# Kernel tuning notes

Hardware: AMD Instinct MI355X
Metric: run time of the kernel (lower is better)

Reference implementation:

```python
import jax, jax.numpy as jnp
import numpy as np

V, E, H, DV = 32000, 512, 1024, 512
B, K = 64, 49


def setup_inputs():
    key = jax.random.key(0)
    ks = jax.random.split(key, 16)
    p = lambda i, shape: jax.random.normal(ks[i], shape, dtype=jnp.float32) * 0.02
    return {
        "thought": jax.random.normal(ks[0], (B, H), dtype=jnp.float32),
        "visual_features": jax.random.normal(ks[1], (B, K, DV), dtype=jnp.float32),
        "max_len": 64,
        "embedding": p(2, (V, E)),
        "Wih1": p(3, (4 * H, E)), "Whh1": p(4, (4 * H, H)),
        "bih1": jnp.zeros((4 * H,), jnp.float32), "bhh1": jnp.zeros((4 * H,), jnp.float32),
        "Wih2": p(5, (4 * H, H)), "Whh2": p(6, (4 * H, H)),
        "bih2": jnp.zeros((4 * H,), jnp.float32), "bhh2": jnp.zeros((4 * H,), jnp.float32),
        "Wg1": p(7, (H, H)), "bg1": jnp.zeros((H,), jnp.float32),
        "Wg2": p(8, (1, H)), "bg2": jnp.zeros((1,), jnp.float32),
        "Wo": p(9, (V, H)), "bo": jnp.zeros((V,), jnp.float32),
        "Wv": p(10, (H, DV)), "bv": jnp.zeros((H,), jnp.float32),
        "ln_g": jnp.ones((H,), jnp.float32), "ln_b": jnp.zeros((H,), jnp.float32),
    }


def _lstm_cell(x, h, c, Wih, Whh, bih, bhh):
    # PyTorch LSTM gate order: i, f, g, o
    z = x @ Wih.T + h @ Whh.T + bih + bhh
    i, f, g, o = jnp.split(z, 4, axis=-1)
    c_new = jax.nn.sigmoid(f) * c + jax.nn.sigmoid(i) * jnp.tanh(g)
    h_new = jax.nn.sigmoid(o) * jnp.tanh(c_new)
    return h_new, c_new


def reference(thought, visual_features, max_len, embedding, Wih1, Whh1, bih1, bhh1,
              Wih2, Whh2, bih2, bbh2=None, bih2_dummy=None, **_unused):
    raise RuntimeError('placeholder')


def reference(thought, visual_features, max_len, embedding, Wih1, Whh1, bih1, bhh1,
              Wih2, Whh2, bih2, bhh2, Wg1, bg1, Wg2, bg2, Wo, bo, Wv, bv, ln_g, ln_b):
    Bsz, Hd = thought.shape
    temperature = 0.4  # epoch = 0 -> 0.4 + 0.4*0
    top_p = 0.7        # epoch = 0 -> 0.7 + 0.2*0
    scale = 1.0 / jnp.sqrt(jnp.asarray(Hd, jnp.float32))
    # visual_proj: Linear + LayerNorm (Dropout is identity in eval mode)
    vp = visual_features @ Wv.T + bv
    mu = vp.mean(-1, keepdims=True)
    var = vp.var(-1, keepdims=True)
    vp = (vp - mu) / jnp.sqrt(var + 1e-5) * ln_g + ln_b  # [B,K,H]
    b_idx = jnp.arange(Bsz)
    # carry: (h1,c1,h2,c2, input token, last-3 token history, history validity)
    init = (thought, jnp.zeros_like(thought), thought, jnp.zeros_like(thought),
            jnp.full((Bsz,), 1, jnp.int32),
            jnp.zeros((Bsz, 3), jnp.int32), jnp.zeros((Bsz, 3), jnp.bool_))
    keys = jax.random.split(jax.random.key(42), max_len)

    def step(carry, key):
        h1, c1, h2, c2, inp, hist, histv = carry
        emb = embedding[inp]  # [B,E]
        h1, c1 = _lstm_cell(emb, h1, c1, Wih1, Whh1, bih1, bhh1)
        h2, c2 = _lstm_cell(h1, h2, c2, Wih2, Whh2, bih2, bhh2)
        gate = jax.nn.sigmoid(jnp.tanh(h2 @ Wg1.T + bg1) @ Wg2.T + bg2)  # [B,1]
        out = h2 * gate
        attn = jax.nn.softmax(jnp.einsum('bh,bkh->bk', out, vp) * scale, axis=-1)
        out = out + jnp.einsum('bk,bkh->bh', attn, vp)
        logits = out @ Wo.T + bo  # [B,V]
        # repetition penalty: -2.0 once per UNIQUE token in last-3 history (set semantics via .max)
        pen = jnp.zeros_like(logits).at[b_idx[:, None], hist].max(histv.astype(logits.dtype))
        logits = (logits - 2.0 * pen) / temperature
        # nucleus (top-p) filtering, matching top_k_top_p_filtering with top_k=0
        order = jnp.argsort(-logits, axis=-1)
        sl = jnp.take_along_axis(logits, order, axis=-1)
        cum = jnp.cumsum(jax.nn.softmax(sl, axis=-1), axis=-1)
        rem = cum > top_p
        rem = jnp.concatenate([jnp.zeros_like(rem[:, :1]), rem[:, :-1]], axis=-1)
        mask = jnp.zeros_like(rem).at[b_idx[:, None], order].set(rem)
        logits = jnp.where(mask, -jnp.inf, logits)
        nxt = jax.random.categorical(key, logits).astype(jnp.int32)  # multinomial sample
        hist = jnp.concatenate([hist[:, 1:], nxt[:, None]], axis=1)
        histv = jnp.concatenate([histv[:, 1:], jnp.ones((Bsz, 1), jnp.bool_)], axis=1)
        return (h1, c1, h2, c2, nxt, hist, histv), nxt

    _, toks = jax.lax.scan(step, init, keys)
    return toks.T  # [B, max_len]
```

## Files before the change

### kernel.cpp

```cpp
#include <hip/hip_runtime.h>
#include <hip/hip_bf16.h>
#include <stdint.h>


#define B_   64
#define H_   1024
#define E_   512
#define DV_  512
#define KV_  49
#define V_   32000
#define T_   64

__device__ __forceinline__ uint32_t rotl32(uint32_t x, int r) {
  return (x << r) | (x >> (32 - r));
}
__device__ __forceinline__ void tf2x32(uint32_t k0, uint32_t k1,
                                       uint32_t x0, uint32_t x1,
                                       uint32_t& o0, uint32_t& o1) {
  uint32_t ks0 = k0, ks1 = k1, ks2 = k0 ^ k1 ^ 0x1BD11BDAu;
  x0 += ks0; x1 += ks1;
#define RND_(r) { x0 += x1; x1 = rotl32(x1, r) ^ x0; }
  RND_(13) RND_(15) RND_(26) RND_(6)  x0 += ks1; x1 += ks2 + 1u;
  RND_(17) RND_(29) RND_(16) RND_(24) x0 += ks2; x1 += ks0 + 2u;
  RND_(13) RND_(15) RND_(26) RND_(6)  x0 += ks0; x1 += ks1 + 3u;
  RND_(17) RND_(29) RND_(16) RND_(24) x0 += ks1; x1 += ks2 + 4u;
  RND_(13) RND_(15) RND_(26) RND_(6)  x0 += ks2; x1 += ks0 + 5u;
#undef RND_
  o0 = x0; o1 = x1;
}

__device__ __forceinline__ unsigned key_of(float f) {
  unsigned u = __float_as_uint(f);
  return (u & 0x80000000u) ? ~u : (u | 0x80000000u);
}
__device__ __forceinline__ float sigf(float x) { return 1.0f / (1.0f + expf(-x)); }

template <int BN, int TM, int TN, int NTHR>
__global__ __launch_bounds__(NTHR)
void gemm_dq(const float* __restrict__ A0, int lda0, const float* __restrict__ W0,
             int ldw0, int K0, float* __restrict__ out0, int ldo0, int nt0,
             const float* __restrict__ A1, int lda1, const float* __restrict__ W1,
             int ldw1, int K1, float* __restrict__ out1, int ldo1) {
  constexpr int LD = 36;
  constexpr int ROWS = 64 + BN;
  constexpr int NF4 = ROWS * 8 / NTHR;
  constexpr int BUFST = ROWS * LD;
  constexpr int CG = BN / TN;
  static_assert(ROWS * 8 % NTHR == 0, "staging divisibility");
  static_assert((64 / TM) * CG == NTHR, "thread grid");
  static_assert(TN == 4, "float4 epilogue");
  __shared__ __align__(16) float S[2][ROWS][LD];

  const int tid = threadIdx.x;
  const int bx = blockIdx.x;
  const float* A; const float* W; float* out;
  int lda, ldw, K, ldo, n0;
  if (bx < nt0) { A = A0; W = W0; out = out0; lda = lda0; ldw = ldw0; K = K0; ldo = ldo0; n0 = bx * BN; }
  else          { A = A1; W = W1; out = out1; lda = lda1; ldw = ldw1; K = K1; ldo = ldo1; n0 = (bx - nt0) * BN; }
  const int m0 = blockIdx.y * 64;
  const int tc = tid % CG, tr = tid / CG;

  const float* gp[NF4];
  float* lp[NF4];
#pragma unroll
  for (int q = 0; q < NF4; ++q) {
    int l = tid + q * NTHR;
    int r = l >> 3, c4 = l & 7;
    gp[q] = (l < 512) ? (A + (m0 + r) * lda + c4 * 4)
                      : (W + (n0 + (r - 64)) * ldw + c4 * 4);
    lp[q] = &S[0][r][(c4 ^ ((r >> 2) & 7)) << 2];
  }

  float4 pre[NF4];
#pragma unroll
  for (int q = 0; q < NF4; ++q) pre[q] = *(const float4*)gp[q];
#pragma unroll
  for (int q = 0; q < NF4; ++q) *(float4*)lp[q] = pre[q];
  __syncthreads();

  float acc[TM][TN] = {};
  const int nch = K >> 5;
  for (int c = 0; c < nch; ++c) {
    const bool more = (c + 1 < nch);
    if (more) {
      const int kc = (c + 1) << 5;
#pragma unroll
      for (int q = 0; q < NF4; ++q) pre[q] = *(const float4*)(gp[q] + kc);
    }
    const float* Sb = &S[c & 1][0][0];
#pragma unroll
    for (int kk = 0; kk < 8; ++kk) {
      float4 a4[TM], w4[TN];
#pragma unroll
      for (int i = 0; i < TM; ++i) {
        int m = tr * TM + i;
        a4[i] = *(const float4*)(Sb + m * LD + ((kk ^ ((m >> 2) & 7)) << 2));
      }
#pragma unroll
      for (int j = 0; j < TN; ++j) {
        int rw = 64 + tc * TN + j;
        w4[j] = *(const float4*)(Sb + rw * LD + ((kk ^ ((rw >> 2) & 7)) << 2));
      }
#pragma unroll
      for (int i = 0; i < TM; ++i)
#pragma unroll
        for (int j = 0; j < TN; ++j) {
          acc[i][j] = fmaf(a4[i].x, w4[j].x, acc[i][j]);
          acc[i][j] = fmaf(a4[i].y, w4[j].y, acc[i][j]);
          acc[i][j] = fmaf(a4[i].z, w4[j].z, acc[i][j]);
          acc[i][j] = fmaf(a4[i].w, w4[j].w, acc[i][j]);
        }
    }
    if (more) {
      const int bo = ((c + 1) & 1) * BUFST;
#pragma unroll
      for (int q = 0; q < NF4; ++q) *(float4*)(lp[q] + bo) = pre[q];
    }
    __syncthreads();
  }

#pragma unroll
  for (int i = 0; i < TM; ++i) {
    float4 o;
    o.x = acc[i][0]; o.y = acc[i][1]; o.z = acc[i][2]; o.w = acc[i][3];
    *(float4*)&out[(m0 + tr * TM + i) * ldo + n0 + tc * TN] = o;
  }
}

__global__ __launch_bounds__(256)
void ln_vp(float* __restrict__ vp, const float* __restrict__ bv,
           const float* __restrict__ g, const float* __restrict__ bt) {
  int row = blockIdx.x, tid = threadIdx.x;
  __shared__ float buf[H_];
  __shared__ float red[256];
  float* p = vp + (long long)row * H_;
  for (int h = tid; h < H_; h += 256) buf[h] = __fadd_rn(p[h], bv[h]);
  __syncthreads();
  float s = 0;
  for (int h = tid; h < H_; h += 256) s += buf[h];
  red[tid] = s; __syncthreads();
  for (int off = 128; off > 0; off >>= 1) { if (tid < off) red[tid] += red[tid + off]; __syncthreads(); }
  float mu = red[0] / (float)H_;
  __syncthreads();
  float vs = 0;
  for (int h = tid; h < H_; h += 256) { float d = buf[h] - mu; vs += d * d; }
  red[tid] = vs; __syncthreads();
  for (int off = 128; off > 0; off >>= 1) { if (tid < off) red[tid] += red[tid + off]; __syncthreads(); }
  float var = red[0] / (float)H_;
  float sq = sqrtf(var + 1e-5f);
  for (int h = tid; h < H_; h += 256) {
    float nrm = __fdiv_rn(__fsub_rn(buf[h], mu), sq);
    p[h] = __fadd_rn(__fmul_rn(nrm, g[h]), bt[h]);
  }
}

__global__ __launch_bounds__(256)
void lstm_cell2(const float* __restrict__ dx, const float* __restrict__ dh,
                const float* __restrict__ bih, const float* __restrict__ bhh,
                float* __restrict__ c,
                float* __restrict__ hA, int ldA, float* __restrict__ hB, int ldB) {
  int idx = blockIdx.x * 256 + threadIdx.x;
  int b = idx >> 10, h = idx & 1023;
  float z[4];
#pragma unroll
  for (int g = 0; g < 4; g++) {
    int j = g * 1024 + h;
    float s = __fadd_rn(dx[b * 4096 + j], dh[b * 4096 + j]);
    s = __fadd_rn(s, bih[j]);
    s = __fadd_rn(s, bhh[j]);
    z[g] = s;
  }
  float fc = __fmul_rn(sigf(z[1]), c[idx]);
  float ig = __fmul_rn(sigf(z[0]), tanhf(z[2]));
  float cn = __fadd_rn(fc, ig);
  float hn = __fmul_rn(sigf(z[3]), tanhf(cn));
  c[idx] = cn;
  hA[(long long)b * ldA + h] = hn;
  hB[(long long)b * ldB + h] = hn;
}

__global__ __launch_bounds__(256)
void gate_attn(const float* __restrict__ dg, const float* __restrict__ bg1,
               const float* __restrict__ Wg2, const float* __restrict__ bg2,
               const float* __restrict__ h2buf, const float* __restrict__ vp,
               float* __restrict__ ctx) {
  int b = blockIdx.x, tid = threadIdx.x;
  __shared__ float t1[H_], outv[H_], attn[64];
  __shared__ float gate_s;
  for (int h = tid; h < H_; h += 256)
    t1[h] = tanhf(__fadd_rn(dg[b * H_ + h], bg1[h]));
  __syncthreads();
  if (tid == 0) {
    float s = 0;
    for (int h = 0; h < H_; h++) s = fmaf(t1[h], Wg2[h], s);
    gate_s = sigf(__fadd_rn(s, bg2[0]));
  }
  __syncthreads();
  float gate = gate_s;
  for (int h = tid; h < H_; h += 256) outv[h] = __fmul_rn(h2buf[b * H_ + h], gate);
  __syncthreads();
  if (tid < KV_) {
    const float* vrow = vp + ((long long)b * KV_ + tid) * H_;
    float a = 0;
    for (int h = 0; h < H_; h++) a = fmaf(outv[h], vrow[h], a);
    attn[tid] = __fmul_rn(a, 0.03125f);
  }
  __syncthreads();
  if (tid == 0) {
    float m = -INFINITY;
    for (int k = 0; k < KV_; k++) m = fmaxf(m, attn[k]);
    float ss = 0;
    for (int k = 0; k < KV_; k++) { attn[k] = expf(attn[k] - m); ss += attn[k]; }
    for (int k = 0; k < KV_; k++) attn[k] = __fdiv_rn(attn[k], ss);
  }
  __syncthreads();
  for (int h = tid; h < H_; h += 256) {
    float acc = 0;
    for (int k = 0; k < KV_; k++) acc = fmaf(attn[k], vp[((long long)b * KV_ + k) * H_ + h], acc);
    ctx[b * H_ + h] = __fadd_rn(outv[h], acc);
  }
}

__global__ __launch_bounds__(256)
void init_state(const float* __restrict__ thought, const float* __restrict__ embedding,
                float* c1, float* c2, float* xcat1, float* xcat2,
                int* hist, int* histv) {
  int i = blockIdx.x * 256 + threadIdx.x;
  if (i < B_ * H_) {
    int b = i >> 10, h = i & 1023;
    c1[i] = 0.f; c2[i] = 0.f;
    float th = thought[i];
    xcat1[b * (E_ + H_) + E_ + h] = th;
    xcat2[b * (2 * H_) + H_ + h] = th;
    if (h < E_) xcat1[b * (E_ + H_) + h] = embedding[E_ + h];
  }
  if (i < B_ * 3) { hist[i] = 0; histv[i] = 0; }
}

__global__ __launch_bounds__(1024)
void sample_kernel(const float* __restrict__ dlog, const float* __restrict__ bo,
                   float* __restrict__ Lbuf, float* __restrict__ Ebuf,
                   int* __restrict__ hist, int* __restrict__ histv,
                   const float* __restrict__ embedding, float* __restrict__ xcat1,
                   int* __restrict__ outTok, int t) {
  int b = blockIdx.x, tid = threadIdx.x;
  __shared__ float redf[1024];
  __shared__ int   redi[1024];
  __shared__ unsigned long long whist[16][257];
  __shared__ unsigned long long binS[256], suf[256];
  __shared__ unsigned long long wq[4];
  __shared__ int jstar_s;
  __shared__ unsigned long long carry_s;
  __shared__ unsigned prefix_s;

  int hh0 = hist[b * 3 + 0], hh1 = hist[b * 3 + 1], hh2 = hist[b * 3 + 2];
  int p0 = histv[b * 3 + 0] ? hh0 : -1;
  int p1 = histv[b * 3 + 1] ? hh1 : -1;
  int p2 = histv[b * 3 + 2] ? hh2 : -1;
  const float* pa = dlog + (long long)b * V_;
  float* L = Lbuf + (long long)b * V_;
  float* E = Ebuf + (long long)b * V_;

  float lm = -INFINITY;
  for (int v = tid; v < V_; v += 1024) {
    float raw = __fadd_rn(pa[v], bo[v]);
    if (v == p0 || v == p1 || v == p2) raw = __fsub_rn(raw, 2.0f);
    float l = __fdiv_rn(raw, 0.4f);
    L[v] = l;
    lm = fmaxf(lm, l);
  }
  redf[tid] = lm; __syncthreads();
  for (int off = 512; off > 0; off >>= 1) { if (tid < off) redf[tid] = fmaxf(redf[tid], redf[tid + off]); __syncthreads(); }
  float m = redf[0];
  __syncthreads();

  float ls = 0;
  for (int v = tid; v < V_; v += 1024) { float e = expf(L[v] - m); E[v] = e; ls += e; }
  redf[tid] = ls; __syncthreads();
  for (int off = 512; off > 0; off >>= 1) { if (tid < off) redf[tid] += redf[tid + off]; __syncthreads(); }
  float Z = redf[0];
  __syncthreads();

  const double SC = 17592186044416.0;
  const unsigned long long B0 =
      (unsigned long long)(0.699999988079071044921875 * 17592186044416.0);
  if (tid == 0) { carry_s = 0ull; prefix_s = 0u; }
  __syncthreads();
  const int lane = tid & 63;
  const int wid = tid >> 6;
  for (int pass = 0; pass < 4; pass++) {
    int shift = 24 - 8 * pass;
    unsigned maskk = (pass == 0) ? 0u : (0xFFFFFFFFu << (shift + 8));
    for (int i = tid; i < 16 * 257; i += 1024) (&whist[0][0])[i] = 0ull;
    __syncthreads();
    unsigned pref = prefix_s;
    unsigned long long carry = carry_s;

    for (int v = tid; v < V_; v += 1024) {
      unsigned key = key_of(L[v]);
      if ((key & maskk) == pref) {
        unsigned bin = (key >> shift) & 255u;
        unsigned long long S = (unsigned long long)((double)(E[v] / Z) * SC);
        atomicAdd(&whist[wid][bin], (S << 16) | 1ull);
      }
    }
    __syncthreads();

    if (tid < 256) {
      unsigned long long s = 0ull;
#pragma unroll
      for (int w = 0; w < 16; ++w) s += whist[w][tid];
      binS[tid] = s;
    }
    if (tid == 0) jstar_s = 256;
    __syncthreads();

    unsigned long long sincl = 0ull, sown = 0ull;
    if (tid < 256) {
      sown = binS[tid] >> 16;
      sincl = sown;
#pragma unroll
      for (int off = 1; off < 64; off <<= 1) {
        unsigned long long o = __shfl_down(sincl, off);
        if (lane + off < 64) sincl += o;
      }
      if (lane == 0) wq[tid >> 6] = sincl;
    }
    __syncthreads();
    if (tid < 256) {
      unsigned long long add = 0ull;
      for (int w2 = (tid >> 6) + 1; w2 < 4; ++w2) add += wq[w2];
      suf[tid] = sincl + add - sown;
    }
    __syncthreads();
    if (tid < 256 && (unsigned)(binS[tid] & 0xFFFFull) > 0u) {
      unsigned long long A = carry + suf[tid];
      if (A <= B0) atomicMin(&jstar_s, tid);
    }
    __syncthreads();
    if (tid == 0) {
      int j = jstar_s;
      carry_s = carry + suf[j];
      prefix_s = pref | (((unsigned)j) << shift);
    }
    __syncthreads();
  }
  unsigned Kstar = prefix_s;

  unsigned kt0, kt1;
  tf2x32(0u, 42u, 0u, (unsigned)t, kt0, kt1);

  float bestv = -INFINITY; int besti = 0x7fffffff;
  for (int v = tid; v < V_; v += 1024) {
    float l = L[v];
    if (key_of(l) >= Kstar) {
      unsigned r0, r1;
      tf2x32(kt0, kt1, 0u, (unsigned)(b * V_ + v), r0, r1);
      unsigned bits = r0 ^ r1;
      float u = __uint_as_float((bits >> 9) | 0x3f800000u) - 1.0f;
      u = fmaxf(u, 1.17549435e-38f);
      float gum = -logf(-logf(u));
      float val = __fadd_rn(l, gum);
      if (val > bestv) { bestv = val; besti = v; }
    }
  }
  redf[tid] = bestv; redi[tid] = besti; __syncthreads();
  for (int off = 512; off > 0; off >>= 1) {
    if (tid < off) {
      float ov = redf[tid + off]; int oi = redi[tid + off];
      if (ov > redf[tid] || (ov == redf[tid] && oi < redi[tid])) { redf[tid] = ov; redi[tid] = oi; }
    }
    __syncthreads();
  }
  int tok = redi[0];
  if (tid == 0) {
    outTok[b * T_ + t] = tok;
    hist[b * 3 + 0] = hh1; hist[b * 3 + 1] = hh2; hist[b * 3 + 2] = tok;
    int v1 = histv[b * 3 + 1], v2 = histv[b * 3 + 2];
    histv[b * 3 + 0] = v1; histv[b * 3 + 1] = v2; histv[b * 3 + 2] = 1;
  }
  for (int k = tid; k < E_; k += 1024)
    xcat1[b * (E_ + H_) + k] = embedding[(long long)tok * E_ + k];
}

extern "C" void kernel_launch(void* const* d_in, const int* in_sizes, int n_in,
                              void* d_out, int out_size, void* d_ws, size_t ws_size,
                              hipStream_t stream) {
  const float* thought   = (const float*)d_in[0];
  const float* visf      = (const float*)d_in[1];
  const float* embedding = (const float*)d_in[3];
  const float* Wih1 = (const float*)d_in[4];
  const float* Whh1 = (const float*)d_in[5];
  const float* bih1 = (const float*)d_in[6];
  const float* bhh1 = (const float*)d_in[7];
  const float* Wih2 = (const float*)d_in[8];
  const float* Whh2 = (const float*)d_in[9];
  const float* bih2 = (const float*)d_in[10];
  const float* bhh2 = (const float*)d_in[11];
  const float* Wg1  = (const float*)d_in[12];
  const float* bg1  = (const float*)d_in[13];
  const float* Wg2  = (const float*)d_in[14];
  const float* bg2  = (const float*)d_in[15];
  const float* Wo   = (const float*)d_in[16];
  const float* bo   = (const float*)d_in[17];
  const float* Wv   = (const float*)d_in[18];
  const float* bv   = (const float*)d_in[19];
  const float* ln_g = (const float*)d_in[20];
  const float* ln_b = (const float*)d_in[21];
  int* outTok = (int*)d_out;

  float* ws = (float*)d_ws;
  long long off = 0;
  float* vp    = ws + off; off += (long long)B_ * KV_ * H_;
  float* xcat1 = ws + off; off += B_ * (E_ + H_);
  float* xcat2 = ws + off; off += B_ * (2 * H_);
  float* c1    = ws + off; off += B_ * H_;
  float* c2    = ws + off; off += B_ * H_;
  float* h2buf = ws + off; off += B_ * H_;
  float* ctx   = ws + off; off += B_ * H_;
  float* dx    = ws + off; off += (long long)B_ * 4096;
  float* dh    = ws + off; off += (long long)B_ * 4096;
  float* dg    = ws + off; off += (long long)B_ * H_;
  float* dlog  = ws + off; off += (long long)B_ * V_;
  float* Lbuf  = ws + off; off += (long long)B_ * V_;
  float* Ebuf  = ws + off; off += (long long)B_ * V_;
  int* hist  = (int*)(ws + off); off += 256;
  int* histv = (int*)(ws + off); off += 256;

  init_state<<<256, 256, 0, stream>>>(thought, embedding, c1, c2, xcat1, xcat2, hist, histv);

  gemm_dq<128, 8, 4, 256><<<dim3(8, KV_), 256, 0, stream>>>(
      visf, DV_, Wv, DV_, DV_, vp, H_, 8,
      visf, DV_, Wv, DV_, DV_, vp, H_);
  ln_vp<<<B_ * KV_, 256, 0, stream>>>(vp, bv, ln_g, ln_b);

  for (int t = 0; t < T_; t++) {
    gemm_dq<32, 4, 4, 128><<<dim3(256, 1), 128, 0, stream>>>(
        xcat1, E_ + H_, Wih1, E_, E_, dx, 4096, 128,
        xcat1 + E_, E_ + H_, Whh1, H_, H_, dh, 4096);
    lstm_cell2<<<256, 256, 0, stream>>>(dx, dh, bih1, bhh1, c1,
                                        xcat1 + E_, E_ + H_, xcat2, 2 * H_);
    gemm_dq<32, 4, 4, 128><<<dim3(256, 1), 128, 0, stream>>>(
        xcat2, 2 * H_, Wih2, H_, H_, dx, 4096, 128,
        xcat2 + H_, 2 * H_, Whh2, H_, H_, dh, 4096);
    lstm_cell2<<<256, 256, 0, stream>>>(dx, dh, bih2, bhh2, c2,
                                        h2buf, H_, xcat2 + H_, 2 * H_);
    gemm_dq<32, 4, 4, 128><<<dim3(32, 1), 128, 0, stream>>>(
        h2buf, H_, Wg1, H_, H_, dg, H_, 32,
        h2buf, H_, Wg1, H_, H_, dg, H_);
    gate_attn<<<B_, 256, 0, stream>>>(dg, bg1, Wg2, bg2, h2buf, vp, ctx);
    gemm_dq<128, 8, 4, 256><<<dim3(250, 1), 256, 0, stream>>>(
        ctx, H_, Wo, H_, H_, dlog, V_, 250,
        ctx, H_, Wo, H_, H_, dlog, V_);
    sample_kernel<<<B_, 1024, 0, stream>>>(dlog, bo, Lbuf, Ebuf, hist, histv,
                                           embedding, xcat1, outTok, t);
  }
}
```

Measured before the change: 30.22 ms.

## Fuse gate GEMM into attention kernel and keep sampling logits in registers

Removes the separate Wg1 GEMM launch by computing h2·Wg1ᵀ inside the gate/attention kernel, using a transposed copy of Wg1 built once in init_state. Sampling now holds the 32 per-thread logits in registers instead of global L/E buffers, recomputing exp in each radix pass, and shrinks the shared histogram from 16 to 8 copies. The fused GEMV does 1024 dependent serial steps per block over only 64 blocks, each re-reading the 4MB weight matrix, which could be slower than the tiled GEMM. The register-resident sampling adds repeated expf work and register pressure.

```diff
diff --git a/kernel.cpp b/kernel.cpp
--- a/kernel.cpp
+++ b/kernel.cpp
@@ -112,9 +112,9 @@
         }
     }
     if (more) {
-      const int bo = ((c + 1) & 1) * BUFST;
-#pragma unroll
-      for (int q = 0; q < NF4; ++q) *(float4*)(lp[q] + bo) = pre[q];
+      const int bo2 = ((c + 1) & 1) * BUFST;
+#pragma unroll
+      for (int q = 0; q < NF4; ++q) *(float4*)(lp[q] + bo2) = pre[q];
     }
     __syncthreads();
   }
@@ -180,15 +180,28 @@
 }
 
 __global__ __launch_bounds__(256)
-void gate_attn(const float* __restrict__ dg, const float* __restrict__ bg1,
-               const float* __restrict__ Wg2, const float* __restrict__ bg2,
-               const float* __restrict__ h2buf, const float* __restrict__ vp,
-               float* __restrict__ ctx) {
+void gate_attn_f(const float* __restrict__ WgT, const float* __restrict__ bg1,
+                 const float* __restrict__ Wg2, const float* __restrict__ bg2,
+                 const float* __restrict__ h2buf, const float* __restrict__ vp,
+                 float* __restrict__ ctx) {
   int b = blockIdx.x, tid = threadIdx.x;
   __shared__ float t1[H_], outv[H_], attn[64];
   __shared__ float gate_s;
-  for (int h = tid; h < H_; h += 256)
-    t1[h] = tanhf(__fadd_rn(dg[b * H_ + h], bg1[h]));
+  {
+    float s0 = 0, s1 = 0, s2 = 0, s3 = 0;
+    for (int k = 0; k < H_; ++k) {
+      float hk = h2buf[b * H_ + k];
+      const float* wr = WgT + k * H_;
+      s0 = fmaf(hk, wr[tid], s0);
+      s1 = fmaf(hk, wr[tid + 256], s1);
+      s2 = fmaf(hk, wr[tid + 512], s2);
+      s3 = fmaf(hk, wr[tid + 768], s3);
+    }
+    t1[tid]       = tanhf(__fadd_rn(s0, bg1[tid]));
+    t1[tid + 256] = tanhf(__fadd_rn(s1, bg1[tid + 256]));
+    t1[tid + 512] = tanhf(__fadd_rn(s2, bg1[tid + 512]));
+    t1[tid + 768] = tanhf(__fadd_rn(s3, bg1[tid + 768]));
+  }
   __syncthreads();
   if (tid == 0) {
     float s = 0;
@@ -223,6 +236,7 @@
 
 __global__ __launch_bounds__(256)
 void init_state(const float* __restrict__ thought, const float* __restrict__ embedding,
+                const float* __restrict__ Wg1, float* __restrict__ WgT,
                 float* c1, float* c2, float* xcat1, float* xcat2,
                 int* hist, int* histv) {
   int i = blockIdx.x * 256 + threadIdx.x;
@@ -235,19 +249,22 @@
     if (h < E_) xcat1[b * (E_ + H_) + h] = embedding[E_ + h];
   }
   if (i < B_ * 3) { hist[i] = 0; histv[i] = 0; }
+  for (int x = i; x < H_ * H_; x += 256 * 256) {
+    int k = x >> 10, j = x & 1023;
+    WgT[x] = Wg1[j * H_ + k];
+  }
 }
 
 __global__ __launch_bounds__(1024)
 void sample_kernel(const float* __restrict__ dlog, const float* __restrict__ bo,
-                   float* __restrict__ Lbuf, float* __restrict__ Ebuf,
                    int* __restrict__ hist, int* __restrict__ histv,
                    const float* __restrict__ embedding, float* __restrict__ xcat1,
                    int* __restrict__ outTok, int t) {
   int b = blockIdx.x, tid = threadIdx.x;
   __shared__ float redf[1024];
   __shared__ int   redi[1024];
-  __shared__ unsigned long long whist[16][257];
-  __shared__ unsigned long long binS[256], suf[256];
+  __shared__ unsigned long long whist[8][257];
+  __shared__ unsigned long long suf[256];
   __shared__ unsigned long long wq[4];
   __shared__ int jstar_s;
   __shared__ unsigned long long carry_s;
@@ -258,16 +275,20 @@
   int p1 = histv[b * 3 + 1] ? hh1 : -1;
   int p2 = histv[b * 3 + 2] ? hh2 : -1;
   const float* pa = dlog + (long long)b * V_;
-  float* L = Lbuf + (long long)b * V_;
-  float* E = Ebuf + (long long)b * V_;
-
+
+  float L[32];
   float lm = -INFINITY;
-  for (int v = tid; v < V_; v += 1024) {
-    float raw = __fadd_rn(pa[v], bo[v]);
-    if (v == p0 || v == p1 || v == p2) raw = __fsub_rn(raw, 2.0f);
-    float l = __fdiv_rn(raw, 0.4f);
-    L[v] = l;
-    lm = fmaxf(lm, l);
+#pragma unroll
+  for (int e = 0; e < 32; ++e) {
+    int v = tid + (e << 10);
+    float l = -INFINITY;
+    if (v < V_) {
+      float raw = __fadd_rn(pa[v], bo[v]);
+      if (v == p0 || v == p1 || v == p2) raw = __fsub_rn(raw, 2.0f);
+      l = __fdiv_rn(raw, 0.4f);
+      lm = fmaxf(lm, l);
+    }
+    L[e] = l;
   }
   redf[tid] = lm; __syncthreads();
   for (int off = 512; off > 0; off >>= 1) { if (tid < off) redf[tid] = fmaxf(redf[tid], redf[tid + off]); __syncthreads(); }
@@ -275,7 +296,11 @@
   __syncthreads();
 
   float ls = 0;
-  for (int v = tid; v < V_; v += 1024) { float e = expf(L[v] - m); E[v] = e; ls += e; }
+#pragma unroll
+  for (int e = 0; e < 32; ++e) {
+    int v = tid + (e << 10);
+    if (v < V_) ls += expf(L[e] - m);
+  }
   redf[tid] = ls; __syncthreads();
   for (int off = 512; off > 0; off >>= 1) { if (tid < off) redf[tid] += redf[tid + off]; __syncthreads(); }
   float Z = redf[0];
@@ -286,45 +311,46 @@
       (unsigned long long)(0.699999988079071044921875 * 17592186044416.0);
   if (tid == 0) { carry_s = 0ull; prefix_s = 0u; }
   __syncthreads();
-  const int lane = tid & 63;
-  const int wid = tid >> 6;
+  const int wid = tid >> 7;
   for (int pass = 0; pass < 4; pass++) {
     int shift = 24 - 8 * pass;
     unsigned maskk = (pass == 0) ? 0u : (0xFFFFFFFFu << (shift + 8));
-    for (int i = tid; i < 16 * 257; i += 1024) (&whist[0][0])[i] = 0ull;
+    for (int i = tid; i < 8 * 257; i += 1024) ((unsigned long long*)whist)[i] = 0ull;
     __syncthreads();
     unsigned pref = prefix_s;
     unsigned long long carry = carry_s;
-
-    for (int v = tid; v < V_; v += 1024) {
-      unsigned key = key_of(L[v]);
-      if ((key & maskk) == pref) {
-        unsigned bin = (key >> shift) & 255u;
-        unsigned long long S = (unsigned long long)((double)(E[v] / Z) * SC);
-        atomicAdd(&whist[wid][bin], (S << 16) | 1ull);
+#pragma unroll
+    for (int e = 0; e < 32; ++e) {
+      int v = tid + (e << 10);
+      if (v < V_) {
+        unsigned key = key_of(L[e]);
+        if ((key & maskk) == pref) {
+          unsigned bin = (key >> shift) & 255u;
+          float ee = expf(L[e] - m);
+          unsigned long long S = (unsigned long long)((double)(ee / Z) * SC);
+          atomicAdd(&whist[wid][bin], (S << 16) | 1ull);
+        }
       }
     }
     __syncthreads();
 
+    unsigned long long bs = 0ull;
     if (tid < 256) {
-      unsigned long long s = 0ull;
-#pragma unroll
-      for (int w = 0; w < 16; ++w) s += whist[w][tid];
-      binS[tid] = s;
+#pragma unroll
+      for (int w = 0; w < 8; ++w) bs += whist[w][tid];
     }
     if (tid == 0) jstar_s = 256;
     __syncthreads();
-
-    unsigned long long sincl = 0ull, sown = 0ull;
+    unsigned long long sown = 0ull, sincl = 0ull;
     if (tid < 256) {
-      sown = binS[tid] >> 16;
+      sown = bs >> 16;
       sincl = sown;
 #pragma unroll
       for (int off = 1; off < 64; off <<= 1) {
         unsigned long long o = __shfl_down(sincl, off);
-        if (lane + off < 64) sincl += o;
+        if ((tid & 63) + off < 64) sincl += o;
       }
-      if (lane == 0) wq[tid >> 6] = sincl;
+      if ((tid & 63) == 0) wq[tid >> 6] = sincl;
     }
     __syncthreads();
     if (tid < 256) {
@@ -333,7 +359,7 @@
       suf[tid] = sincl + add - sown;
     }
     __syncthreads();
-    if (tid < 256 && (unsigned)(binS[tid] & 0xFFFFull) > 0u) {
+    if (tid < 256 && (unsigned)(bs & 0xFFFFull) > 0u) {
       unsigned long long A = carry + suf[tid];
       if (A <= B0) atomicMin(&jstar_s, tid);
     }
@@ -351,17 +377,21 @@
   tf2x32(0u, 42u, 0u, (unsigned)t, kt0, kt1);
 
   float bestv = -INFINITY; int besti = 0x7fffffff;
-  for (int v = tid; v < V_; v += 1024) {
-    float l = L[v];
-    if (key_of(l) >= Kstar) {
-      unsigned r0, r1;
-      tf2x32(kt0, kt1, 0u, (unsigned)(b * V_ + v), r0, r1);
-      unsigned bits = r0 ^ r1;
-      float u = __uint_as_float((bits >> 9) | 0x3f800000u) - 1.0f;
-      u = fmaxf(u, 1.17549435e-38f);
-      float gum = -logf(-logf(u));
-      float val = __fadd_rn(l, gum);
-      if (val > bestv) { bestv = val; besti = v; }
+#pragma unroll
+  for (int e = 0; e < 32; ++e) {
+    int v = tid + (e << 10);
+    if (v < V_) {
+      float l = L[e];
+      if (key_of(l) >= Kstar) {
+        unsigned r0, r1;
+        tf2x32(kt0, kt1, 0u, (unsigned)(b * V_ + v), r0, r1);
+        unsigned bits = r0 ^ r1;
+        float u = __uint_as_float((bits >> 9) | 0x3f800000u) - 1.0f;
+        u = fmaxf(u, 1.17549435e-38f);
+        float gum = -logf(-logf(u));
+        float val = __fadd_rn(l, gum);
+        if (val > bestv) { bestv = val; besti = v; }
+      }
     }
   }
   redf[tid] = bestv; redi[tid] = besti; __syncthreads();
@@ -420,14 +450,13 @@
   float* ctx   = ws + off; off += B_ * H_;
   float* dx    = ws + off; off += (long long)B_ * 4096;
   float* dh    = ws + off; off += (long long)B_ * 4096;
-  float* dg    = ws + off; off += (long long)B_ * H_;
   float* dlog  = ws + off; off += (long long)B_ * V_;
-  float* Lbuf  = ws + off; off += (long long)B_ * V_;
-  float* Ebuf  = ws + off; off += (long long)B_ * V_;
+  float* WgT   = ws + off; off += (long long)H_ * H_;
   int* hist  = (int*)(ws + off); off += 256;
   int* histv = (int*)(ws + off); off += 256;
 
-  init_state<<<256, 256, 0, stream>>>(thought, embedding, c1, c2, xcat1, xcat2, hist, histv);
+  init_state<<<256, 256, 0, stream>>>(thought, embedding, Wg1, WgT,
+                                      c1, c2, xcat1, xcat2, hist, histv);
 
   gemm_dq<128, 8, 4, 256><<<dim3(8, KV_), 256, 0, stream>>>(
       visf, DV_, Wv, DV_, DV_, vp, H_, 8,
@@ -445,14 +474,11 @@
         xcat2 + H_, 2 * H_, Whh2, H_, H_, dh, 4096);
     lstm_cell2<<<256, 256, 0, stream>>>(dx, dh, bih2, bhh2, c2,
                                         h2buf, H_, xcat2 + H_, 2 * H_);
-    gemm_dq<32, 4, 4, 128><<<dim3(32, 1), 128, 0, stream>>>(
-        h2buf, H_, Wg1, H_, H_, dg, H_, 32,
-        h2buf, H_, Wg1, H_, H_, dg, H_);
-    gate_attn<<<B_, 256, 0, stream>>>(dg, bg1, Wg2, bg2, h2buf, vp, ctx);
+    gate_attn_f<<<B_, 256, 0, stream>>>(WgT, bg1, Wg2, bg2, h2buf, vp, ctx);
     gemm_dq<128, 8, 4, 256><<<dim3(250, 1), 256, 0, stream>>>(
         ctx, H_, Wo, H_, H_, dlog, V_, 250,
         ctx, H_, Wo, H_, H_, dlog, V_);
-    sample_kernel<<<B_, 1024, 0, stream>>>(dlog, bo, Lbuf, Ebuf, hist, histv,
+    sample_kernel<<<B_, 1024, 0, stream>>>(dlog, bo, hist, histv,
                                            embedding, xcat1, outTok, t);
   }
 }
```

Measured after the change: 29.83 ms. No clear change (-1.3%).
